# Performance work log

Hardware: AMD Instinct MI355X
Metric: run time of the kernel (lower is better)

The kernel has to match this reference:

```python
import jax, jax.numpy as jnp
import numpy as np

# NOTE: the original source calls an undefined selective_scan_fn(x, delta, A_bar, B_bar, C)
# and returns y_proj(y). We implement the standard S6 diagonal selective scan it implies:
#   h_t = A_bar_t * h_{t-1} + B_bar_t * u_t   (elementwise over latent dim, h_0 = 0)
#   y_t = C_t * h_t
# with u = x_proj(x) (the only use of the otherwise-dangling x_proj in the source).

IN_CH = 96
OUT_CH = 96
LATENT = 256
BATCH, H, W = 2, 128, 128


def _linear(x, w, b):
    return x @ w.T + b


def _s6(x, xw, xb, bcw, bcb, dw, db, yw, yb):
    # x: [B, L, Cin]
    u = _linear(x, xw, xb)                      # [B, L, D]
    bc = _linear(x, bcw, bcb)                   # [B, L, 2D]
    delta = _linear(x, dw, db)                  # [B, L, D]
    Bm, Cm = jnp.split(bc, 2, axis=-1)
    A_bar = jnp.exp(-jax.nn.softplus(delta))    # in (0, 1)
    B_bar = (1.0 - A_bar) * Bm
    elems = (A_bar, B_bar * u)

    def combine(c1, c2):
        a1, b1 = c1
        a2, b2 = c2
        return (a1 * a2, a2 * b1 + b2)

    _, h = jax.lax.associative_scan(combine, elems, axis=1)  # parallel scan over L
    y = Cm * h
    return _linear(y, yw, yb)                   # [B, L, D]


def setup_inputs() -> dict:
    key = jax.random.key(0)
    ks = jax.random.split(key, 16)
    s = 0.02
    inp = {
        "x": jax.random.normal(ks[0], (BATCH, IN_CH, H, W), jnp.float32),
        # S6 params (shared across all 4 directional scans, as in the source)
        "xw": jax.random.normal(ks[1], (LATENT, IN_CH), jnp.float32) * s,
        "xb": jnp.zeros((LATENT,), jnp.float32),
        "bcw": jax.random.normal(ks[2], (2 * LATENT, IN_CH), jnp.float32) * s,
        "bcb": jnp.zeros((2 * LATENT,), jnp.float32),
        "dw": jax.random.normal(ks[3], (LATENT, IN_CH), jnp.float32) * s,
        "db": jnp.zeros((LATENT,), jnp.float32),
        "yw": jax.random.normal(ks[4], (LATENT, LATENT), jnp.float32) * s,
        "yb": jnp.zeros((LATENT,), jnp.float32),
        # CrossMerge params
        "mw": jax.random.normal(ks[5], (LATENT, 4 * LATENT), jnp.float32) * s,
        "mb": jnp.zeros((LATENT,), jnp.float32),
        "gw": jax.random.normal(ks[6], (LATENT, 4 * LATENT), jnp.float32) * s,
        "gb": jnp.zeros((LATENT,), jnp.float32),
        "ow": jax.random.normal(ks[7], (OUT_CH, LATENT), jnp.float32) * s,
        "ob": jnp.zeros((OUT_CH,), jnp.float32),
    }
    return inp


def reference(x, xw, xb, bcw, bcb, dw, db, yw, yb, mw, mb, gw, gb, ow, ob):
    B, C, Hh, Ww = x.shape
    # cross_scan: 4 directional flattenings
    s1 = x.transpose(0, 2, 3, 1).reshape(B, Hh * Ww, C)   # 'b c h w -> b (h w) c'
    s2 = x.transpose(0, 3, 2, 1).reshape(B, Ww * Hh, C)   # 'b c h w -> b (w h) c'
    s3 = s1[:, ::-1, :]
    s4 = s2[:, ::-1, :]
    p = (xw, xb, bcw, bcb, dw, db, yw, yb)
    y1 = _s6(s1, *p)
    y2 = _s6(s2, *p)
    y3 = _s6(s3, *p)
    y4 = _s6(s4, *p)
    # CrossMerge
    y_cat = jnp.concatenate([y1, y2, y3, y4], axis=-1)    # [B, L, 4D]
    y_merged = _linear(y_cat, mw, mb)
    gate = jax.nn.sigmoid(_linear(y_cat, gw, gb))
    out = _linear(y_merged * gate, ow, ob)                # [B, L, OUT_CH]
    # 'b (h w) c -> b c h w'
    return out.reshape(B, Hh, Ww, -1).transpose(0, 3, 1, 2)
```

## Files before the change

kernel.cpp:

```cpp
#include <hip/hip_runtime.h>
#include <stdint.h>

#define LL 16384
#define NB 2
#define CIN 96
#define NLAT 256
#define COUT 96

typedef __attribute__((ext_vector_type(8))) short short8v;
typedef __attribute__((ext_vector_type(4))) float float4v;

__device__ __forceinline__ float b2f(unsigned short h) {
    return __uint_as_float(((unsigned int)h) << 16);
}
__device__ __forceinline__ unsigned short f2b(float f) {
    unsigned int u = __float_as_uint(f);
    unsigned int r = (u + 0x7FFFu + ((u >> 16) & 1u)) >> 16;
    return (unsigned short)r;
}

#define GLL16(g, s) __builtin_amdgcn_global_load_lds( \
    (const __attribute__((address_space(1))) unsigned int*)(g), \
    (__attribute__((address_space(3))) unsigned int*)(s), 16, 0, 0)

__global__ __launch_bounds__(256) void k_foldw_part(
    const float* __restrict__ yw, const float* __restrict__ mw, const float* __restrict__ gw,
    float* __restrict__ WF)
{
    __shared__ float At[64][68];
    __shared__ float Bt[64][68];
    int jt = blockIdx.x, nt = blockIdx.y, dzk = blockIdx.z;
    int kc = dzk & 3, dz = dzk >> 2;
    int d = dz & 3, mat = dz >> 2;
    const float* src = mat ? gw : mw;
    int j0 = jt * 64, n0 = nt * 64;
    int tid = threadIdx.x, tx = tid & 15, ty = tid >> 4;
    float acc[4][4] = {};
    int i0 = kc * 64;
    for (int rep = 0; rep < 16; ++rep) {
        int idx = rep * 256 + tid;
        int r = idx >> 6, cq = idx & 63;
        At[r][cq] = yw[(size_t)(i0 + r) * 256 + j0 + cq];
        Bt[cq][r] = src[(size_t)(n0 + r) * 1024 + d * 256 + i0 + cq];
    }
    __syncthreads();
    for (int ii = 0; ii < 64; ++ii) {
        float4 a4 = *(const float4*)(&At[ii][ty * 4]);
        float4 b4 = *(const float4*)(&Bt[ii][tx * 4]);
        float av[4] = {a4.x, a4.y, a4.z, a4.w};
        float bv[4] = {b4.x, b4.y, b4.z, b4.w};
        for (int q = 0; q < 4; ++q)
            for (int p = 0; p < 4; ++p)
                acc[q][p] = fmaf(av[q], bv[p], acc[q][p]);
    }
    float* dst = WF + (size_t)kc * 512 * 1024;
    for (int q = 0; q < 4; ++q) {
        int k = d * 256 + j0 + ty * 4 + q;
        for (int p = 0; p < 4; ++p) {
            int n = n0 + tx * 4 + p;
            dst[(size_t)(mat * 256 + n) * 1024 + k] = acc[q][p];
        }
    }
}

__global__ __launch_bounds__(256) void k_foldsum(
    const float* __restrict__ WF, unsigned short* __restrict__ WBT)
{
    int t = blockIdx.x * 256 + threadIdx.x;
    size_t o = (size_t)t * 4;
    const size_t S = (size_t)512 * 1024;
    float4 s0 = *(const float4*)(WF + o);
    float4 s1 = *(const float4*)(WF + S + o);
    float4 s2 = *(const float4*)(WF + 2 * S + o);
    float4 s3 = *(const float4*)(WF + 3 * S + o);
    unsigned short pk[4];
    pk[0] = f2b(s0.x + s1.x + s2.x + s3.x);
    pk[1] = f2b(s0.y + s1.y + s2.y + s3.y);
    pk[2] = f2b(s0.z + s1.z + s2.z + s3.z);
    pk[3] = f2b(s0.w + s1.w + s2.w + s3.w);
    *(unsigned long long*)(&WBT[o]) = *(const unsigned long long*)pk;
}

__global__ void k_foldbias(const float* __restrict__ mw, const float* __restrict__ gw,
                           const float* __restrict__ mb, const float* __restrict__ gb,
                           const float* __restrict__ yb,
                           float* __restrict__ bm2, float* __restrict__ bg2)
{
    int row = blockIdx.x;
    int lane = threadIdx.x;
    int n = row & 255;
    const float* W = (row < 256) ? mw : gw;
    float s = 0.f;
    for (int k = lane; k < 1024; k += 64)
        s = fmaf(W[(size_t)n * 1024 + k], yb[k & 255], s);
    for (int off = 32; off; off >>= 1) s += __shfl_down(s, off);
    if (lane == 0) {
        if (row < 256) bm2[n] = s + mb[n];
        else           bg2[n] = s + gb[n];
    }
}

__global__ __launch_bounds__(256) void k_xpose(
    const float* __restrict__ x, unsigned short* __restrict__ XT)
{
    int t = threadIdx.x;
    int pl = t & 63;
    int grp = t >> 6;
    int p0 = blockIdx.x * 64;
    int b = p0 >> 14;
    int l = (p0 & (LL - 1)) + pl;
    size_t gp = (size_t)(p0 + pl);
    const float* xr = x + (size_t)b * 96 * LL + l;
    unsigned short* orow = XT + gp * 192;
#pragma unroll
    for (int kk = 0; kk < 3; ++kk) {
        int kq = grp * 3 + kk;
        short8v hi, lo;
#pragma unroll
        for (int c = 0; c < 8; ++c) {
            float v = xr[(size_t)(kq * 8 + c) * LL];
            unsigned short h = f2b(v);
            float r = v - b2f(h);
            hi[c] = (short)h;
            lo[c] = (short)f2b(r);
        }
        *(short8v*)(orow + kq * 8) = hi;
        *(short8v*)(orow + 96 + kq * 8) = lo;
    }
}

__global__ void k_wprep(
    const float* __restrict__ xw, const float* __restrict__ bcw, const float* __restrict__ dw,
    unsigned short* __restrict__ WPT)
{
    int rp = blockIdx.x * 32 + (threadIdx.x >> 3);
    int sub = threadIdx.x & 7;
    int nn16 = rp >> 6, g = (rp >> 4) & 3, ni = rp & 15;
    int n = nn16 * 16 + ni;
    const float* row;
    if (g == 0)      row = xw + (size_t)n * 96;
    else if (g == 1) row = bcw + (size_t)n * 96;
    else if (g == 2) row = bcw + (size_t)(256 + n) * 96;
    else             row = dw + (size_t)n * 96;
    unsigned short* orow = WPT + (size_t)rp * 192;
    for (int kq = sub; kq < 12; kq += 8) {
        short8v hv;
#pragma unroll
        for (int c = 0; c < 8; ++c) hv[c] = (short)f2b(row[kq * 8 + c]);
        *(short8v*)(orow + kq * 8) = hv;
        *(short8v*)(orow + 96 + kq * 8) = hv;
    }
}

__global__ void k_owprep(const float* __restrict__ ow, unsigned short* __restrict__ OWB)
{
    int r = blockIdx.x;
    int lane = threadIdx.x;
    unsigned short pk[4];
    if (r < 96) {
        float4 v = *(const float4*)(ow + (size_t)r * 256 + lane * 4);
        pk[0] = f2b(v.x); pk[1] = f2b(v.y); pk[2] = f2b(v.z); pk[3] = f2b(v.w);
    } else {
        pk[0] = pk[1] = pk[2] = pk[3] = 0;
    }
    *(unsigned long long*)(&OWB[(size_t)r * 256 + lane * 4]) = *(const unsigned long long*)pk;
}

__global__ __launch_bounds__(256) void k_proj_mfma(
    const unsigned short* __restrict__ XT, const unsigned short* __restrict__ WPT,
    const float* __restrict__ xb, const float* __restrict__ bcb, const float* __restrict__ db,
    unsigned int* __restrict__ AB, unsigned short* __restrict__ C)
{
    __shared__ __align__(16) unsigned short smA[128 * 32];
    __shared__ __align__(16) unsigned short smB[128 * 32];
    int tid = threadIdx.x;
    int w = tid >> 6, l = tid & 63;
    int mt = blockIdx.x;
    int bnt = blockIdx.y;
    int p0 = mt * 128;
    int bn0 = bnt * 128;

    int rowA = tid >> 2;
    int chA  = tid & 3;
    int laneRow = l & 15;
    int laneK   = l >> 4;

    float4v acc[2][8];
#pragma unroll
    for (int i = 0; i < 2; ++i)
#pragma unroll
        for (int f = 0; f < 8; ++f) acc[i][f] = (float4v)0.f;

    for (int kt = 0; kt < 6; ++kt) {
        const unsigned short* gA = XT + (size_t)(p0 + rowA) * 192 + kt * 32 + chA * 8;
        const unsigned short* gB = WPT + (size_t)(bn0 + rowA) * 192 + kt * 32 + chA * 8;
        GLL16(gA,            smA + tid * 8);
        GLL16(gA + 64 * 192, smA + 2048 + tid * 8);
        GLL16(gB,            smB + tid * 8);
        GLL16(gB + 64 * 192, smB + 2048 + tid * 8);
        __syncthreads();

        short8v a0 = *(const short8v*)(&smA[(w * 32 + laneRow) * 32 + laneK * 8]);
        short8v a1 = *(const short8v*)(&smA[(w * 32 + 16 + laneRow) * 32 + laneK * 8]);
#pragma unroll
        for (int f = 0; f < 8; ++f) {
            short8v bf_ = *(const short8v*)(&smB[(f * 16 + laneRow) * 32 + laneK * 8]);
            acc[0][f] = __builtin_amdgcn_mfma_f32_16x16x32_bf16(a0, bf_, acc[0][f], 0, 0, 0);
            acc[1][f] = __builtin_amdgcn_mfma_f32_16x16x32_bf16(a1, bf_, acc[1][f], 0, 0, 0);
        }
        __syncthreads();
    }

    int lr = l >> 4, lc = l & 15;
#pragma unroll
    for (int mr = 0; mr < 2; ++mr) {
#pragma unroll
        for (int nn2 = 0; nn2 < 2; ++nn2) {
            int n = (bnt * 2 + nn2) * 16 + lc;
            float xbv = xb[n], bb = bcb[n], cb = bcb[256 + n], dbv = db[n];
#pragma unroll
            for (int q = 0; q < 4; ++q) {
                int p = p0 + w * 32 + mr * 16 + lr * 4 + q;
                float u  = acc[mr][nn2 * 4 + 0][q] + xbv;
                float Bm = acc[mr][nn2 * 4 + 1][q] + bb;
                float Cm = acc[mr][nn2 * 4 + 2][q] + cb;
                float dl = acc[mr][nn2 * 4 + 3][q] + dbv;
                float a  = 1.0f / (1.0f + __expf(dl));
                float bu = (1.0f - a) * Bm * u;
                size_t base = (size_t)p * NLAT + n;
                AB[base] = (unsigned int)f2b(a) | ((unsigned int)f2b(bu) << 16);
                C[base]  = f2b(Cm);
            }
        }
    }
}

__device__ __forceinline__ int src_pos(int d, int t) {
    int s = (d >= 2) ? (LL - 1 - t) : t;
    return (d & 1) ? (((s & 127) << 7) | (s >> 7)) : s;
}

__global__ __launch_bounds__(256) void k_scan1(
    const unsigned int* __restrict__ AB,
    float* __restrict__ AggA, float* __restrict__ AggB)
{
    int n = threadIdx.x;
    int c = blockIdx.x, d = blockIdx.y, b = blockIdx.z;
    float h = 0.f, Ap = 1.f;
    int t0 = c * 256;
#pragma unroll 4
    for (int i = 0; i < 256; ++i) {
        int ls = src_pos(d, t0 + i);
        unsigned int v = AB[((size_t)b * LL + ls) * NLAT + n];
        float a  = __uint_as_float(v << 16);
        float bu = __uint_as_float(v & 0xFFFF0000u);
        h = fmaf(a, h, bu);
        Ap *= a;
    }
    size_t o = (((size_t)b * 4 + d) * 64 + c) * NLAT + n;
    AggA[o] = Ap; AggB[o] = h;
}

__global__ void k_scan2(const float* __restrict__ AggA, const float* __restrict__ AggB,
                        float* __restrict__ Hs)
{
    int n = threadIdx.x;
    int d = blockIdx.x, b = blockIdx.y;
    float h = 0.f;
    for (int c = 0; c < 64; ++c) {
        size_t o = (((size_t)b * 4 + d) * 64 + c) * NLAT + n;
        Hs[o] = h;
        h = fmaf(AggA[o], h, AggB[o]);
    }
}

__global__ __launch_bounds__(256) void k_scan3(
    const unsigned int* __restrict__ AB, const unsigned short* __restrict__ C,
    const float* __restrict__ Hs, unsigned short* __restrict__ ys)
{
    int n = threadIdx.x;
    int c = blockIdx.x, d = blockIdx.y, b = blockIdx.z;
    size_t o = (((size_t)b * 4 + d) * 64 + c) * NLAT + n;
    float h = Hs[o];
    int t0 = c * 256;
    size_t ybase = (((size_t)b * 4 + d) * LL + t0) * NLAT + n;
#pragma unroll 4
    for (int i = 0; i < 256; ++i) {
        int ls = src_pos(d, t0 + i);
        size_t idx = ((size_t)b * LL + ls) * NLAT + n;
        unsigned int v = AB[idx];
        float a  = __uint_as_float(v << 16);
        float bu = __uint_as_float(v & 0xFFFF0000u);
        h = fmaf(a, h, bu);
        float y = b2f(C[idx]) * h;
        ys[ybase + (size_t)i * NLAT] = f2b(y);
    }
}

__global__ __launch_bounds__(256) void k_merge_mfma(
    const unsigned short* __restrict__ ys,
    const unsigned short* __restrict__ WBT,
    const float* __restrict__ bm2, const float* __restrict__ bg2,
    unsigned short* __restrict__ z)
{
    __shared__ __align__(16) unsigned short smA[2 * 128 * 32];
    __shared__ __align__(16) unsigned short smB[2 * 256 * 32];
    int tid = threadIdx.x;
    int w = tid >> 6, l = tid & 63;
    int wm = w >> 1, wn = w & 1;
    int mt = blockIdx.x;
    int nt = blockIdx.y;
    int p0 = mt * 128;
    int b4 = (p0 >> 14) * 4;
    int l0 = p0 & (LL - 1);
    int n0 = nt * 128;

    int rS = tid >> 2;
    int cg = (tid & 3) ^ ((rS >> 1) & 3);
    int laneRow = l & 15;
    int laneK   = l >> 4;
    int rx = (laneRow >> 1) & 3;

    float4v accM[4][4], accG[4][4];
#pragma unroll
    for (int i = 0; i < 4; ++i)
#pragma unroll
        for (int j = 0; j < 4; ++j) { accM[i][j] = (float4v)0.f; accG[i][j] = (float4v)0.f; }

    auto stage = [&](int kt, int buf) {
        int d = kt >> 3;
        int j0k = (kt & 7) * 32;
        const unsigned short* gAb = ys + (((size_t)(b4 + d)) * LL + l0) * 256 + j0k + cg * 8;
        unsigned short* sA = smA + buf * 4096;
        unsigned short* sB = smB + buf * 8192;
#pragma unroll
        for (int rep = 0; rep < 2; ++rep) {
            GLL16(gAb + (size_t)(rep * 64 + rS) * 256, sA + rep * 2048 + tid * 8);
        }
#pragma unroll
        for (int rep = 0; rep < 4; ++rep) {
            int rr = rep * 64 + rS;
            int nrow = (rr < 128) ? (n0 + rr) : (256 + n0 + rr - 128);
            GLL16(WBT + (size_t)nrow * 1024 + kt * 32 + cg * 8, sB + rep * 2048 + tid * 8);
        }
    };

    stage(0, 0);

    int cur = 0;
    for (int kt = 0; kt < 32; ++kt) {
        if (kt < 31) {
            stage(kt + 1, cur ^ 1);
            asm volatile("s_waitcnt vmcnt(6)" ::: "memory");
        } else {
            asm volatile("s_waitcnt vmcnt(0)" ::: "memory");
        }
        __builtin_amdgcn_s_barrier();

        const unsigned short* sA = smA + cur * 4096;
        const unsigned short* sB = smB + cur * 8192;
        int cxo = (laneK ^ rx) * 8;
        short8v a[4];
#pragma unroll
        for (int mr = 0; mr < 4; ++mr)
            a[mr] = *(const short8v*)(&sA[(wm * 64 + mr * 16 + laneRow) * 32 + cxo]);
#pragma unroll
        for (int nr = 0; nr < 4; ++nr) {
            short8v bm_ = *(const short8v*)(&sB[(wn * 64 + nr * 16 + laneRow) * 32 + cxo]);
            short8v bg_ = *(const short8v*)(&sB[(128 + wn * 64 + nr * 16 + laneRow) * 32 + cxo]);
#pragma unroll
            for (int mr = 0; mr < 4; ++mr) {
                accM[mr][nr] = __builtin_amdgcn_mfma_f32_16x16x32_bf16(a[mr], bm_, accM[mr][nr], 0, 0, 0);
                accG[mr][nr] = __builtin_amdgcn_mfma_f32_16x16x32_bf16(a[mr], bg_, accG[mr][nr], 0, 0, 0);
            }
        }
        __builtin_amdgcn_s_barrier();
        cur ^= 1;
    }

    int lr = l >> 4, lc = l & 15;
#pragma unroll
    for (int mr = 0; mr < 4; ++mr) {
#pragma unroll
        for (int nr = 0; nr < 4; ++nr) {
            int n = n0 + wn * 64 + nr * 16 + lc;
            float bmv = bm2[n], bgv = bg2[n];
#pragma unroll
            for (int q = 0; q < 4; ++q) {
                int p = p0 + wm * 64 + mr * 16 + lr * 4 + q;
                float m = accM[mr][nr][q] + bmv;
                float g = accG[mr][nr][q] + bgv;
                float zv = m / (1.f + __expf(-g));
                z[(size_t)p * NLAT + n] = f2b(zv);
            }
        }
    }
}

__global__ __launch_bounds__(256) void k_out_mfma(
    const unsigned short* __restrict__ z, const unsigned short* __restrict__ OWB,
    const float* __restrict__ ob, float* __restrict__ out)
{
    __shared__ __align__(16) unsigned short smA[128 * 32];
    __shared__ __align__(16) unsigned short smB[128 * 32];
    int tid = threadIdx.x;
    int w = tid >> 6, l = tid & 63;
    int p0 = blockIdx.x * 128;
    int b = p0 >> 14;
    int l0 = p0 & (LL - 1);

    int rowA = tid >> 2;
    int chA  = tid & 3;
    int laneRow = l & 15;
    int laneK   = l >> 4;

    float4v acc[2][6];
#pragma unroll
    for (int i = 0; i < 2; ++i)
#pragma unroll
        for (int f = 0; f < 6; ++f) acc[i][f] = (float4v)0.f;

    for (int kt = 0; kt < 8; ++kt) {
        const unsigned short* gA = z + (size_t)(p0 + rowA) * 256 + kt * 32 + chA * 8;
        const unsigned short* gB = OWB + (size_t)rowA * 256 + kt * 32 + chA * 8;
        GLL16(gA,            smA + tid * 8);
        GLL16(gA + 64 * 256, smA + 2048 + tid * 8);
        GLL16(gB,            smB + tid * 8);
        GLL16(gB + 64 * 256, smB + 2048 + tid * 8);
        __syncthreads();

        short8v a0 = *(const short8v*)(&smA[(w * 32 + laneRow) * 32 + laneK * 8]);
        short8v a1 = *(const short8v*)(&smA[(w * 32 + 16 + laneRow) * 32 + laneK * 8]);
#pragma unroll
        for (int nr = 0; nr < 6; ++nr) {
            short8v bf_ = *(const short8v*)(&smB[(nr * 16 + laneRow) * 32 + laneK * 8]);
            acc[0][nr] = __builtin_amdgcn_mfma_f32_16x16x32_bf16(a0, bf_, acc[0][nr], 0, 0, 0);
            acc[1][nr] = __builtin_amdgcn_mfma_f32_16x16x32_bf16(a1, bf_, acc[1][nr], 0, 0, 0);
        }
        __syncthreads();
    }

    int lr = l >> 4, lc = l & 15;
#pragma unroll
    for (int mr = 0; mr < 2; ++mr) {
#pragma unroll
        for (int nr = 0; nr < 6; ++nr) {
            int c = nr * 16 + lc;
            float obv = ob[c];
            int ll = l0 + w * 32 + mr * 16 + lr * 4;
            float4 v;
            v.x = acc[mr][nr][0] + obv;
            v.y = acc[mr][nr][1] + obv;
            v.z = acc[mr][nr][2] + obv;
            v.w = acc[mr][nr][3] + obv;
            *(float4*)(&out[((size_t)(b * 96 + c)) * LL + ll]) = v;
        }
    }
}

extern "C" void kernel_launch(void* const* d_in, const int* in_sizes, int n_in,
                              void* d_out, int out_size, void* d_ws, size_t ws_size,
                              hipStream_t stream) {
    (void)in_sizes; (void)n_in; (void)out_size; (void)ws_size;
    const float* x   = (const float*)d_in[0];
    const float* xw  = (const float*)d_in[1];
    const float* xb  = (const float*)d_in[2];
    const float* bcw = (const float*)d_in[3];
    const float* bcb = (const float*)d_in[4];
    const float* dw  = (const float*)d_in[5];
    const float* db  = (const float*)d_in[6];
    const float* yw  = (const float*)d_in[7];
    const float* yb  = (const float*)d_in[8];
    const float* mw  = (const float*)d_in[9];
    const float* mb  = (const float*)d_in[10];
    const float* gw  = (const float*)d_in[11];
    const float* gb  = (const float*)d_in[12];
    const float* ow  = (const float*)d_in[13];
    const float* ob  = (const float*)d_in[14];
    float* out = (float*)d_out;

    char* ws = (char*)d_ws;
    size_t off = 0;
    auto alloc = [&](size_t bytes) -> void* {
        void* p = ws + off;
        off += (bytes + 255) & ~(size_t)255;
        return p;
    };
    unsigned int*   AB  = (unsigned int*)  alloc((size_t)NB * LL * NLAT * 4);
    unsigned short* C   = (unsigned short*)alloc((size_t)NB * LL * NLAT * 2);
    unsigned short* YS  = (unsigned short*)alloc((size_t)NB * 4 * LL * NLAT * 2);
    unsigned short* Z   = (unsigned short*)alloc((size_t)NB * LL * NLAT * 2);
    unsigned short* WBT = (unsigned short*)alloc((size_t)512 * 1024 * 2);
    unsigned short* XT  = (unsigned short*)alloc((size_t)NB * LL * 192 * 2);
    unsigned short* WPT = (unsigned short*)alloc((size_t)1024 * 192 * 2);
    unsigned short* OWB = (unsigned short*)alloc((size_t)128 * 256 * 2);
    float* WF   = (float*)alloc((size_t)4 * 512 * 1024 * 4);
    float* BM2  = (float*)alloc(256 * 4);
    float* BG2  = (float*)alloc(256 * 4);
    float* AggA = (float*)alloc((size_t)NB * 4 * 64 * NLAT * 4);
    float* AggB = (float*)alloc((size_t)NB * 4 * 64 * NLAT * 4);
    float* HS   = (float*)alloc((size_t)NB * 4 * 64 * NLAT * 4);

    k_foldw_part<<<dim3(4, 4, 32),  256, 0, stream>>>(yw, mw, gw, WF);
    k_foldsum   <<<512,             256, 0, stream>>>(WF, WBT);
    k_foldbias  <<<512,              64, 0, stream>>>(mw, gw, mb, gb, yb, BM2, BG2);
    k_wprep     <<<32,              256, 0, stream>>>(xw, bcw, dw, WPT);
    k_owprep    <<<128,              64, 0, stream>>>(ow, OWB);
    k_xpose     <<<512,             256, 0, stream>>>(x, XT);
    k_proj_mfma <<<dim3(256, 8),    256, 0, stream>>>(XT, WPT, xb, bcb, db, AB, C);
    k_scan1     <<<dim3(64, 4, NB), 256, 0, stream>>>(AB, AggA, AggB);
    k_scan2     <<<dim3(4, NB),     256, 0, stream>>>(AggA, AggB, HS);
    k_scan3     <<<dim3(64, 4, NB), 256, 0, stream>>>(AB, C, HS, YS);
    k_merge_mfma<<<dim3(256, 2),    256, 0, stream>>>(YS, WBT, BM2, BG2, Z);
    k_out_mfma  <<<256,             256, 0, stream>>>(Z, OWB, ob, out);
}
```

Baseline: 191.8 us.

## Pair forward and reversed scan directions per block to share AB chunk reads

The chunked scan now uses 128 chunks of 128 steps. Each block handles direction d and its reverse d+2 over the same source positions, walking the mirrored chunk so both passes touch the same AB/C data. The intent is for the second pass to hit in cache, which halves effective global traffic in scan1 and scan3. The trade-off is that scan2's sequential carry pass becomes twice as long, and each block does its two passes one after the other.

```diff
diff --git a/kernel.cpp b/kernel.cpp
--- a/kernel.cpp
+++ b/kernel.cpp
@@ -6,6 +6,7 @@
 #define CIN 96
 #define NLAT 256
 #define COUT 96
+#define NCH 128
 
 typedef __attribute__((ext_vector_type(8))) short short8v;
 typedef __attribute__((ext_vector_type(4))) float float4v;
@@ -245,20 +246,40 @@
     float* __restrict__ AggA, float* __restrict__ AggB)
 {
     int n = threadIdx.x;
-    int c = blockIdx.x, d = blockIdx.y, b = blockIdx.z;
-    float h = 0.f, Ap = 1.f;
-    int t0 = c * 256;
+    int c = blockIdx.x, dp = blockIdx.y, b = blockIdx.z;
+    {
+        int d = dp;
+        int t0 = c * 128;
+        float h = 0.f, Ap = 1.f;
 #pragma unroll 4
-    for (int i = 0; i < 256; ++i) {
-        int ls = src_pos(d, t0 + i);
-        unsigned int v = AB[((size_t)b * LL + ls) * NLAT + n];
-        float a  = __uint_as_float(v << 16);
-        float bu = __uint_as_float(v & 0xFFFF0000u);
-        h = fmaf(a, h, bu);
-        Ap *= a;
-    }
-    size_t o = (((size_t)b * 4 + d) * 64 + c) * NLAT + n;
-    AggA[o] = Ap; AggB[o] = h;
+        for (int i = 0; i < 128; ++i) {
+            int ls = src_pos(d, t0 + i);
+            unsigned int v = AB[((size_t)b * LL + ls) * NLAT + n];
+            float a  = __uint_as_float(v << 16);
+            float bu = __uint_as_float(v & 0xFFFF0000u);
+            h = fmaf(a, h, bu);
+            Ap *= a;
+        }
+        size_t o = (((size_t)b * 4 + d) * NCH + c) * NLAT + n;
+        AggA[o] = Ap; AggB[o] = h;
+    }
+    {
+        int d = dp + 2;
+        int c2 = NCH - 1 - c;
+        int t0 = c2 * 128;
+        float h = 0.f, Ap = 1.f;
+#pragma unroll 4
+        for (int i = 0; i < 128; ++i) {
+            int ls = src_pos(d, t0 + i);
+            unsigned int v = AB[((size_t)b * LL + ls) * NLAT + n];
+            float a  = __uint_as_float(v << 16);
+            float bu = __uint_as_float(v & 0xFFFF0000u);
+            h = fmaf(a, h, bu);
+            Ap *= a;
+        }
+        size_t o = (((size_t)b * 4 + d) * NCH + c2) * NLAT + n;
+        AggA[o] = Ap; AggB[o] = h;
+    }
 }
 
 __global__ void k_scan2(const float* __restrict__ AggA, const float* __restrict__ AggB,
@@ -267,8 +288,8 @@
     int n = threadIdx.x;
     int d = blockIdx.x, b = blockIdx.y;
     float h = 0.f;
-    for (int c = 0; c < 64; ++c) {
-        size_t o = (((size_t)b * 4 + d) * 64 + c) * NLAT + n;
+    for (int c = 0; c < NCH; ++c) {
+        size_t o = (((size_t)b * 4 + d) * NCH + c) * NLAT + n;
         Hs[o] = h;
         h = fmaf(AggA[o], h, AggB[o]);
     }
@@ -279,21 +300,43 @@
     const float* __restrict__ Hs, unsigned short* __restrict__ ys)
 {
     int n = threadIdx.x;
-    int c = blockIdx.x, d = blockIdx.y, b = blockIdx.z;
-    size_t o = (((size_t)b * 4 + d) * 64 + c) * NLAT + n;
-    float h = Hs[o];
-    int t0 = c * 256;
-    size_t ybase = (((size_t)b * 4 + d) * LL + t0) * NLAT + n;
+    int c = blockIdx.x, dp = blockIdx.y, b = blockIdx.z;
+    {
+        int d = dp;
+        int t0 = c * 128;
+        size_t o = (((size_t)b * 4 + d) * NCH + c) * NLAT + n;
+        float h = Hs[o];
+        size_t ybase = (((size_t)b * 4 + d) * LL + t0) * NLAT + n;
 #pragma unroll 4
-    for (int i = 0; i < 256; ++i) {
-        int ls = src_pos(d, t0 + i);
-        size_t idx = ((size_t)b * LL + ls) * NLAT + n;
-        unsigned int v = AB[idx];
-        float a  = __uint_as_float(v << 16);
-        float bu = __uint_as_float(v & 0xFFFF0000u);
-        h = fmaf(a, h, bu);
-        float y = b2f(C[idx]) * h;
-        ys[ybase + (size_t)i * NLAT] = f2b(y);
+        for (int i = 0; i < 128; ++i) {
+            int ls = src_pos(d, t0 + i);
+            size_t idx = ((size_t)b * LL + ls) * NLAT + n;
+            unsigned int v = AB[idx];
+            float a  = __uint_as_float(v << 16);
+            float bu = __uint_as_float(v & 0xFFFF0000u);
+            h = fmaf(a, h, bu);
+            float y = b2f(C[idx]) * h;
+            ys[ybase + (size_t)i * NLAT] = f2b(y);
+        }
+    }
+    {
+        int d = dp + 2;
+        int c2 = NCH - 1 - c;
+        int t0 = c2 * 128;
+        size_t o = (((size_t)b * 4 + d) * NCH + c2) * NLAT + n;
+        float h = Hs[o];
+        size_t ybase = (((size_t)b * 4 + d) * LL + t0) * NLAT + n;
+#pragma unroll 4
+        for (int i = 0; i < 128; ++i) {
+            int ls = src_pos(d, t0 + i);
+            size_t idx = ((size_t)b * LL + ls) * NLAT + n;
+            unsigned int v = AB[idx];
+            float a  = __uint_as_float(v << 16);
+            float bu = __uint_as_float(v & 0xFFFF0000u);
+            h = fmaf(a, h, bu);
+            float y = b2f(C[idx]) * h;
+            ys[ybase + (size_t)i * NLAT] = f2b(y);
+        }
     }
 }
 
@@ -497,20 +540,20 @@
     float* WF   = (float*)alloc((size_t)4 * 512 * 1024 * 4);
     float* BM2  = (float*)alloc(256 * 4);
     float* BG2  = (float*)alloc(256 * 4);
-    float* AggA = (float*)alloc((size_t)NB * 4 * 64 * NLAT * 4);
-    float* AggB = (float*)alloc((size_t)NB * 4 * 64 * NLAT * 4);
-    float* HS   = (float*)alloc((size_t)NB * 4 * 64 * NLAT * 4);
-
-    k_foldw_part<<<dim3(4, 4, 32),  256, 0, stream>>>(yw, mw, gw, WF);
-    k_foldsum   <<<512,             256, 0, stream>>>(WF, WBT);
-    k_foldbias  <<<512,              64, 0, stream>>>(mw, gw, mb, gb, yb, BM2, BG2);
-    k_wprep     <<<32,              256, 0, stream>>>(xw, bcw, dw, WPT);
-    k_owprep    <<<128,              64, 0, stream>>>(ow, OWB);
-    k_xpose     <<<512,             256, 0, stream>>>(x, XT);
-    k_proj_mfma <<<dim3(256, 8),    256, 0, stream>>>(XT, WPT, xb, bcb, db, AB, C);
-    k_scan1     <<<dim3(64, 4, NB), 256, 0, stream>>>(AB, AggA, AggB);
-    k_scan2     <<<dim3(4, NB),     256, 0, stream>>>(AggA, AggB, HS);
-    k_scan3     <<<dim3(64, 4, NB), 256, 0, stream>>>(AB, C, HS, YS);
-    k_merge_mfma<<<dim3(256, 2),    256, 0, stream>>>(YS, WBT, BM2, BG2, Z);
-    k_out_mfma  <<<256,             256, 0, stream>>>(Z, OWB, ob, out);
-}
+    float* AggA = (float*)alloc((size_t)NB * 4 * NCH * NLAT * 4);
+    float* AggB = (float*)alloc((size_t)NB * 4 * NCH * NLAT * 4);
+    float* HS   = (float*)alloc((size_t)NB * 4 * NCH * NLAT * 4);
+
+    k_foldw_part<<<dim3(4, 4, 32),   256, 0, stream>>>(yw, mw, gw, WF);
+    k_foldsum   <<<512,              256, 0, stream>>>(WF, WBT);
+    k_foldbias  <<<512,               64, 0, stream>>>(mw, gw, mb, gb, yb, BM2, BG2);
+    k_wprep     <<<32,               256, 0, stream>>>(xw, bcw, dw, WPT);
+    k_owprep    <<<128,               64, 0, stream>>>(ow, OWB);
+    k_xpose     <<<512,              256, 0, stream>>>(x, XT);
+    k_proj_mfma <<<dim3(256, 8),     256, 0, stream>>>(XT, WPT, xb, bcb, db, AB, C);
+    k_scan1     <<<dim3(NCH, 2, NB), 256, 0, stream>>>(AB, AggA, AggB);
+    k_scan2     <<<dim3(4, NB),      256, 0, stream>>>(AggA, AggB, HS);
+    k_scan3     <<<dim3(NCH, 2, NB), 256, 0, stream>>>(AB, C, HS, YS);
+    k_merge_mfma<<<dim3(256, 2),     256, 0, stream>>>(YS, WBT, BM2, BG2, Z);
+    k_out_mfma  <<<256,              256, 0, stream>>>(Z, OWB, ob, out);
+}
```

Measured after the change: 192.6 us. Within noise of the previous version (+0.4%).

## Pair forward/reverse scan directions per block and shrink scan chunks

Applied to the files above, without the earlier changes.

The chunked scan now uses 256 chunks of 64 steps instead of 64 chunks of 256, which gives more blocks and shorter serial chains. Each block processes a forward direction together with its reversed counterpart on the mirrored chunk. Both directions read the same AB/C elements, so the second read should hit in cache, and the two independent recurrences interleave to hide latency. In exchange, the serial inter-chunk pass (k_scan2) is four times longer and the aggregate buffers grow.

```diff
diff --git a/kernel.cpp b/kernel.cpp
--- a/kernel.cpp
+++ b/kernel.cpp
@@ -6,6 +6,8 @@
 #define CIN 96
 #define NLAT 256
 #define COUT 96
+#define NCH 256
+#define CHU 64
 
 typedef __attribute__((ext_vector_type(8))) short short8v;
 typedef __attribute__((ext_vector_type(4))) float float4v;
@@ -245,20 +247,27 @@
     float* __restrict__ AggA, float* __restrict__ AggB)
 {
     int n = threadIdx.x;
-    int c = blockIdx.x, d = blockIdx.y, b = blockIdx.z;
-    float h = 0.f, Ap = 1.f;
-    int t0 = c * 256;
+    int c = blockIdx.x, dp = blockIdx.y, b = blockIdx.z;
+    int d1 = dp, d2 = dp + 2;
+    int c2 = NCH - 1 - c;
+    int t01 = c * CHU, t02 = c2 * CHU;
+    const unsigned int* ABb = AB + (size_t)b * LL * NLAT + n;
+    float h1 = 0.f, A1 = 1.f, h2 = 0.f, A2 = 1.f;
 #pragma unroll 4
-    for (int i = 0; i < 256; ++i) {
-        int ls = src_pos(d, t0 + i);
-        unsigned int v = AB[((size_t)b * LL + ls) * NLAT + n];
-        float a  = __uint_as_float(v << 16);
-        float bu = __uint_as_float(v & 0xFFFF0000u);
-        h = fmaf(a, h, bu);
-        Ap *= a;
-    }
-    size_t o = (((size_t)b * 4 + d) * 64 + c) * NLAT + n;
-    AggA[o] = Ap; AggB[o] = h;
+    for (int i = 0; i < CHU; ++i) {
+        int ls1 = src_pos(d1, t01 + i);
+        int ls2 = src_pos(d2, t02 + i);
+        unsigned int v1 = ABb[(size_t)ls1 * NLAT];
+        unsigned int v2 = ABb[(size_t)ls2 * NLAT];
+        float a1 = __uint_as_float(v1 << 16), bu1 = __uint_as_float(v1 & 0xFFFF0000u);
+        float a2 = __uint_as_float(v2 << 16), bu2 = __uint_as_float(v2 & 0xFFFF0000u);
+        h1 = fmaf(a1, h1, bu1); A1 *= a1;
+        h2 = fmaf(a2, h2, bu2); A2 *= a2;
+    }
+    size_t o1 = (((size_t)b * 4 + d1) * NCH + c) * NLAT + n;
+    size_t o2 = (((size_t)b * 4 + d2) * NCH + c2) * NLAT + n;
+    AggA[o1] = A1; AggB[o1] = h1;
+    AggA[o2] = A2; AggB[o2] = h2;
 }
 
 __global__ void k_scan2(const float* __restrict__ AggA, const float* __restrict__ AggB,
@@ -267,8 +276,8 @@
     int n = threadIdx.x;
     int d = blockIdx.x, b = blockIdx.y;
     float h = 0.f;
-    for (int c = 0; c < 64; ++c) {
-        size_t o = (((size_t)b * 4 + d) * 64 + c) * NLAT + n;
+    for (int c = 0; c < NCH; ++c) {
+        size_t o = (((size_t)b * 4 + d) * NCH + c) * NLAT + n;
         Hs[o] = h;
         h = fmaf(AggA[o], h, AggB[o]);
     }
@@ -279,21 +288,32 @@
     const float* __restrict__ Hs, unsigned short* __restrict__ ys)
 {
     int n = threadIdx.x;
-    int c = blockIdx.x, d = blockIdx.y, b = blockIdx.z;
-    size_t o = (((size_t)b * 4 + d) * 64 + c) * NLAT + n;
-    float h = Hs[o];
-    int t0 = c * 256;
-    size_t ybase = (((size_t)b * 4 + d) * LL + t0) * NLAT + n;
+    int c = blockIdx.x, dp = blockIdx.y, b = blockIdx.z;
+    int d1 = dp, d2 = dp + 2;
+    int c2 = NCH - 1 - c;
+    int t01 = c * CHU, t02 = c2 * CHU;
+    const unsigned int* ABb = AB + (size_t)b * LL * NLAT + n;
+    const unsigned short* Cb = C + (size_t)b * LL * NLAT + n;
+    size_t o1 = (((size_t)b * 4 + d1) * NCH + c) * NLAT + n;
+    size_t o2 = (((size_t)b * 4 + d2) * NCH + c2) * NLAT + n;
+    float h1 = Hs[o1], h2 = Hs[o2];
+    size_t yb1 = (((size_t)b * 4 + d1) * LL + t01) * NLAT + n;
+    size_t yb2 = (((size_t)b * 4 + d2) * LL + t02) * NLAT + n;
 #pragma unroll 4
-    for (int i = 0; i < 256; ++i) {
-        int ls = src_pos(d, t0 + i);
-        size_t idx = ((size_t)b * LL + ls) * NLAT + n;
-        unsigned int v = AB[idx];
-        float a  = __uint_as_float(v << 16);
-        float bu = __uint_as_float(v & 0xFFFF0000u);
-        h = fmaf(a, h, bu);
-        float y = b2f(C[idx]) * h;
-        ys[ybase + (size_t)i * NLAT] = f2b(y);
+    for (int i = 0; i < CHU; ++i) {
+        int ls1 = src_pos(d1, t01 + i);
+        int ls2 = src_pos(d2, t02 + i);
+        size_t i1 = (size_t)ls1 * NLAT, i2 = (size_t)ls2 * NLAT;
+        unsigned int v1 = ABb[i1];
+        unsigned int v2 = ABb[i2];
+        float a1 = __uint_as_float(v1 << 16), bu1 = __uint_as_float(v1 & 0xFFFF0000u);
+        float a2 = __uint_as_float(v2 << 16), bu2 = __uint_as_float(v2 & 0xFFFF0000u);
+        h1 = fmaf(a1, h1, bu1);
+        h2 = fmaf(a2, h2, bu2);
+        float y1 = b2f(Cb[i1]) * h1;
+        float y2 = b2f(Cb[i2]) * h2;
+        ys[yb1 + (size_t)i * NLAT] = f2b(y1);
+        ys[yb2 + (size_t)i * NLAT] = f2b(y2);
     }
 }
 
@@ -497,20 +517,20 @@
     float* WF   = (float*)alloc((size_t)4 * 512 * 1024 * 4);
     float* BM2  = (float*)alloc(256 * 4);
     float* BG2  = (float*)alloc(256 * 4);
-    float* AggA = (float*)alloc((size_t)NB * 4 * 64 * NLAT * 4);
-    float* AggB = (float*)alloc((size_t)NB * 4 * 64 * NLAT * 4);
-    float* HS   = (float*)alloc((size_t)NB * 4 * 64 * NLAT * 4);
-
-    k_foldw_part<<<dim3(4, 4, 32),  256, 0, stream>>>(yw, mw, gw, WF);
-    k_foldsum   <<<512,             256, 0, stream>>>(WF, WBT);
-    k_foldbias  <<<512,              64, 0, stream>>>(mw, gw, mb, gb, yb, BM2, BG2);
-    k_wprep     <<<32,              256, 0, stream>>>(xw, bcw, dw, WPT);
-    k_owprep    <<<128,              64, 0, stream>>>(ow, OWB);
-    k_xpose     <<<512,             256, 0, stream>>>(x, XT);
-    k_proj_mfma <<<dim3(256, 8),    256, 0, stream>>>(XT, WPT, xb, bcb, db, AB, C);
-    k_scan1     <<<dim3(64, 4, NB), 256, 0, stream>>>(AB, AggA, AggB);
-    k_scan2     <<<dim3(4, NB),     256, 0, stream>>>(AggA, AggB, HS);
-    k_scan3     <<<dim3(64, 4, NB), 256, 0, stream>>>(AB, C, HS, YS);
-    k_merge_mfma<<<dim3(256, 2),    256, 0, stream>>>(YS, WBT, BM2, BG2, Z);
-    k_out_mfma  <<<256,             256, 0, stream>>>(Z, OWB, ob, out);
-}
+    float* AggA = (float*)alloc((size_t)NB * 4 * NCH * NLAT * 4);
+    float* AggB = (float*)alloc((size_t)NB * 4 * NCH * NLAT * 4);
+    float* HS   = (float*)alloc((size_t)NB * 4 * NCH * NLAT * 4);
+
+    k_foldw_part<<<dim3(4, 4, 32),   256, 0, stream>>>(yw, mw, gw, WF);
+    k_foldsum   <<<512,              256, 0, stream>>>(WF, WBT);
+    k_foldbias  <<<512,               64, 0, stream>>>(mw, gw, mb, gb, yb, BM2, BG2);
+    k_wprep     <<<32,               256, 0, stream>>>(xw, bcw, dw, WPT);
+    k_owprep    <<<128,               64, 0, stream>>>(ow, OWB);
+    k_xpose     <<<512,              256, 0, stream>>>(x, XT);
+    k_proj_mfma <<<dim3(256, 8),     256, 0, stream>>>(XT, WPT, xb, bcb, db, AB, C);
+    k_scan1     <<<dim3(NCH, 2, NB), 256, 0, stream>>>(AB, AggA, AggB);
+    k_scan2     <<<dim3(4, NB),      256, 0, stream>>>(AggA, AggB, HS);
+    k_scan3     <<<dim3(NCH, 2, NB), 256, 0, stream>>>(AB, C, HS, YS);
+    k_merge_mfma<<<dim3(256, 2),     256, 0, stream>>>(YS, WBT, BM2, BG2, Z);
+    k_out_mfma  <<<256,              256, 0, stream>>>(Z, OWB, ob, out);
+}
```

Result: no change. 189.5 us (-1.2%).
